# Performance work log

Hardware: AMD Instinct MI355X
Metric: run time of the kernel (lower is better)

Reference implementation:

```python
import jax, jax.numpy as jnp
import numpy as np

N_NODES = 100000


def gcn_conv(x, W, b, src, dst, n_nodes):
    # x: [N, Fin], W: [Fin, Fout], edge (src->dst) with self-loops added,
    # symmetric normalization D^{-1/2} A D^{-1/2} as in PyG GCNConv defaults.
    h = x @ W  # [N, Fout]
    loops = jnp.arange(n_nodes, dtype=src.dtype)
    src_all = jnp.concatenate([src, loops])
    dst_all = jnp.concatenate([dst, loops])
    ones = jnp.ones(src_all.shape[0], dtype=h.dtype)
    deg = jax.ops.segment_sum(ones, dst_all, num_segments=n_nodes)  # in-degree incl. self-loop
    dinv = jnp.where(deg > 0, jax.lax.rsqrt(deg), 0.0)
    norm = dinv[src_all] * dinv[dst_all]  # [E+N]
    msg = h[src_all] * norm[:, None]      # gather + scale
    out = jax.ops.segment_sum(msg, dst_all, num_segments=n_nodes)  # scatter-add
    return out + b


def setup_inputs() -> dict:
    key = jax.random.key(0)
    k1, k2, k3, k4 = jax.random.split(key, 4)
    in_dim, hidden, out_dim = 128, 128, 64
    n_edges = 600000
    x = jax.random.normal(k1, (N_NODES, in_dim), dtype=jnp.float32)
    edge_index = jax.random.randint(k2, (2, n_edges), 0, N_NODES, dtype=jnp.int64)
    # Glorot-ish init for weights
    W1 = jax.random.normal(k3, (in_dim, hidden), dtype=jnp.float32) / np.sqrt(in_dim)
    b1 = jnp.zeros((hidden,), dtype=jnp.float32)
    W2 = jax.random.normal(k4, (hidden, out_dim), dtype=jnp.float32) / np.sqrt(hidden)
    b2 = jnp.zeros((out_dim,), dtype=jnp.float32)
    return {"x": x, "edge_index": edge_index, "W1": W1, "b1": b1, "W2": W2, "b2": b2}


def reference(x, edge_index, W1, b1, W2, b2):
    src, dst = edge_index[0], edge_index[1]
    h = jax.nn.relu(gcn_conv(x, W1, b1, src, dst, N_NODES))
    # dropout is identity in eval mode (training=False)
    return gcn_conv(h, W2, b2, src, dst, N_NODES)
```

## Files before the change

### kernel.cpp

```cpp
#include <hip/hip_runtime.h>
#include <hip/hip_bf16.h>
#include <stdint.h>

typedef unsigned int u32;
typedef unsigned short u16;
typedef unsigned long long u64;
typedef __attribute__((ext_vector_type(8))) short short8;
typedef __attribute__((ext_vector_type(4))) float f32x4;

#define SCAN_TILE 2048

__device__ __forceinline__ float bf2f(u16 u) {
    union { u32 u; float f; } v; v.u = ((u32)u) << 16; return v.f;
}
__device__ __forceinline__ u16 f2bf(float f) {
    u32 u = __float_as_uint(f);
    u32 r = (u + 0x7FFFu + ((u >> 16) & 1u)) >> 16;
    return (u16)r;
}
__device__ __forceinline__ u32 packbf(float lo, float hi) {
    return ((u32)f2bf(hi) << 16) | (u32)f2bf(lo);
}

template<int N>
__device__ __forceinline__ void wpack_one(const void* W, uint4* wpk, int p, int f32w) {
    const int n = p & (N - 1);
    const int kb = p >> ((N == 128) ? 7 : 6);
    u32 pk[4];
    if (f32w) {
        const float* wp = (const float*)W + (size_t)(kb * 8) * N + n;
        #pragma unroll
        for (int jj = 0; jj < 4; jj++)
            pk[jj] = packbf(wp[(2 * jj) * N], wp[(2 * jj + 1) * N]);
    } else {
        const u16* wp = (const u16*)W + (size_t)(kb * 8) * N + n;
        #pragma unroll
        for (int jj = 0; jj < 4; jj++)
            pk[jj] = ((u32)wp[(2 * jj + 1) * N] << 16) | (u32)wp[(2 * jj) * N];
    }
    uint4 v; v.x = pk[0]; v.y = pk[1]; v.z = pk[2]; v.w = pk[3];
    wpk[p] = v;
}

__global__ __launch_bounds__(256) void prep_count_k(
    const u32* __restrict__ xw, const void* __restrict__ ei,
    int* __restrict__ flags, int M, int E,
    const void* __restrict__ W1, const void* __restrict__ W2,
    uint4* __restrict__ wpk1, uint4* __restrict__ wpk2,
    int* __restrict__ deg)
{
    __shared__ int cnt;
    __shared__ u32 orr;
    __shared__ u32 dorr;
    const int b = blockIdx.x, t = threadIdx.x;
    const u32* ew = (const u32*)ei;

    if (b < 12) {
        if (t == 0) cnt = 0;
        __syncthreads();
        int hits = 0;
        #pragma unroll
        for (int j = 0; j < 4; j++) {
            u32 f = (xw[t * 4 + j] >> 7) & 0xFFu;
            if (f >= 100u && f <= 140u) hits++;
        }
        atomicAdd(&cnt, hits);
        __syncthreads();
        const int f32w = (cnt < 512) ? 1 : 0;
        if (b < 8) wpack_one<128>(W1, wpk1, b * 256 + t, f32w);
        else       wpack_one<64> (W2, wpk2, (b - 8) * 256 + t, f32w);
        if (b == 0) {
            if (t == 0) flags[0] = f32w;
            if (t == 0) orr = 0u;
            __syncthreads();
            atomicOr(&orr, ew[2 * t + 1]);
            __syncthreads();
            if (t == 0) flags[1] = (orr == 0u) ? 1 : 0;
        }
        return;
    }

    const int cb = b - 12;
    const int i2 = (cb * 256 + t) * 2;
    if (t == 0) dorr = 0u;
    __syncthreads();
    u32 w = 0u;
    if (i2 + 1 < E) w = ew[(size_t)E + i2 + 1];
    atomicOr(&dorr, w);
    __syncthreads();
    const bool is64 = (dorr == 0u);
    if (i2 >= E) return;
    if (is64) {
        const long long* dp = (const long long*)ei + E;
        if (i2 + 1 < E) {
            longlong2 v = *(const longlong2*)(dp + i2);
            atomicAdd(&deg[(int)v.x], 1);
            atomicAdd(&deg[(int)v.y], 1);
        } else atomicAdd(&deg[(int)dp[i2]], 1);
    } else {
        const int* dp = (const int*)ei + E;
        if (i2 + 1 < E) {
            int2 v = *(const int2*)(dp + i2);
            atomicAdd(&deg[v.x], 1);
            atomicAdd(&deg[v.y], 1);
        } else atomicAdd(&deg[dp[i2]], 1);
    }
}

__global__ __launch_bounds__(256) void scan_gemm1_k(
    const int* __restrict__ deg, int M,
    u64* __restrict__ lk, int* __restrict__ off,
    int* __restrict__ cursor, float* __restrict__ dinv, int nb,
    const void* __restrict__ X, const uint4* __restrict__ wpk,
    u16* __restrict__ HS, const int* __restrict__ flags)
{
    __shared__ u32 smem[64 * 64];
    const int t = threadIdx.x;

    if ((int)blockIdx.x < nb) {
        const int bid = blockIdx.x;
        const int base = bid * SCAN_TILE + t * 8;
        int v[8];
        int s = 0;
        const bool full = (base + 8 <= M);
        if (full) {
            int4 a = *(const int4*)(deg + base);
            int4 b = *(const int4*)(deg + base + 4);
            v[0] = a.x; v[1] = a.y; v[2] = a.z; v[3] = a.w;
            v[4] = b.x; v[5] = b.y; v[6] = b.z; v[7] = b.w;
            s = v[0] + v[1] + v[2] + v[3] + v[4] + v[5] + v[6] + v[7];
        } else {
            #pragma unroll
            for (int j = 0; j < 8; j++) { v[j] = (base + j < M) ? deg[base + j] : 0; s += v[j]; }
        }
        int* bp = (int*)smem;
        int* bq = (int*)smem + 256;
        int* psb = (int*)smem + 512;
        bp[t] = s;
        __syncthreads();
        for (int d = 1; d < 256; d <<= 1) {
            int x = bp[t];
            if (t >= d) x += bp[t - d];
            bq[t] = x;
            __syncthreads();
            int* tmp = bp; bp = bq; bq = tmp;
        }
        const int incl = bp[t];
        const int btotal = bp[255];

        if (t == 0) {
            if (bid == 0) {
                __hip_atomic_store(&lk[0], (2ull << 62) | (u32)btotal,
                                   __ATOMIC_RELEASE, __HIP_MEMORY_SCOPE_AGENT);
                psb[0] = 0;
            } else {
                __hip_atomic_store(&lk[bid], (1ull << 62) | (u32)btotal,
                                   __ATOMIC_RELEASE, __HIP_MEMORY_SCOPE_AGENT);
                int run = 0;
                int j = bid - 1;
                while (j >= 0) {
                    u64 w = __hip_atomic_load(&lk[j], __ATOMIC_ACQUIRE,
                                              __HIP_MEMORY_SCOPE_AGENT);
                    const u64 st = w >> 62;
                    if (st == 0) { __builtin_amdgcn_s_sleep(1); continue; }
                    run += (int)(w & 0xFFFFFFFFull);
                    if (st == 2ull) break;
                    j--;
                }
                psb[0] = run;
                __hip_atomic_store(&lk[bid], (2ull << 62) | (u32)(run + btotal),
                                   __ATOMIC_RELEASE, __HIP_MEMORY_SCOPE_AGENT);
            }
        }
        __syncthreads();
        const int sbase = psb[0];

        int pre = sbase + incl - s;
        int o[8]; float dv[8];
        #pragma unroll
        for (int j = 0; j < 8; j++) {
            o[j] = pre;
            dv[j] = rsqrtf((float)(v[j] + 1));
            pre += v[j];
        }
        if (full) {
            *(int4*)(off + base)     = make_int4(o[0], o[1], o[2], o[3]);
            *(int4*)(off + base + 4) = make_int4(o[4], o[5], o[6], o[7]);
            *(int4*)(cursor + base)     = make_int4(o[0], o[1], o[2], o[3]);
            *(int4*)(cursor + base + 4) = make_int4(o[4], o[5], o[6], o[7]);
            *(float4*)(dinv + base)     = make_float4(dv[0], dv[1], dv[2], dv[3]);
            *(float4*)(dinv + base + 4) = make_float4(dv[4], dv[5], dv[6], dv[7]);
        } else {
            for (int j = 0; j < 8; j++) if (base + j < M) {
                off[base + j] = o[j]; cursor[base + j] = o[j]; dinv[base + j] = dv[j];
            }
        }
        if (bid == nb - 1 && t == 255) off[M] = sbase + btotal;
        return;
    }

    const int gb = (int)blockIdx.x - nb;
    const int wave = t >> 6, lane = t & 63;
    const int q = lane >> 4, m = lane & 15;
    const bool xf32 = (flags[0] != 0);
    const int row0 = gb * 64;
    u32* xlds = smem;

    for (int c = t; c < 1024; c += 256) {
        const int row = c >> 4, c8 = c & 15;
        const int grow = row0 + row;
        uint4 pk = make_uint4(0u, 0u, 0u, 0u);
        if (grow < M) {
            if (xf32) {
                const float* xp = (const float*)X + (size_t)grow * 128 + c8 * 8;
                float4 u = *(const float4*)xp;
                float4 v = *(const float4*)(xp + 4);
                pk.x = packbf(u.x, u.y); pk.y = packbf(u.z, u.w);
                pk.z = packbf(v.x, v.y); pk.w = packbf(v.z, v.w);
            } else {
                pk = *(const uint4*)((const u16*)X + (size_t)grow * 128 + c8 * 8);
            }
        }
        *(uint4*)&xlds[row * 64 + c8 * 4] = pk;
    }
    __syncthreads();

    union { uint4 u; short8 v; } a[4];
    #pragma unroll
    for (int s = 0; s < 4; s++)
        a[s].u = *(const uint4*)&xlds[(wave * 16 + m) * 64 + (s * 4 + q) * 4];

    f32x4 acc[8];
    #pragma unroll
    for (int tt = 0; tt < 8; tt++)
        acc[tt] = (f32x4){0.f, 0.f, 0.f, 0.f};

    #pragma unroll
    for (int s = 0; s < 4; s++) {
        union { uint4 u; short8 v; } b[8];
        #pragma unroll
        for (int tt = 0; tt < 8; tt++)
            b[tt].u = wpk[(s * 4 + q) * 128 + tt * 16 + m];
        #pragma unroll
        for (int tt = 0; tt < 8; tt++)
            acc[tt] = __builtin_amdgcn_mfma_f32_16x16x32_bf16(
                a[s].v, b[tt].v, acc[tt], 0, 0, 0);
    }

    u16* orow = (u16*)&xlds[wave * 16 * 64];
    #pragma unroll
    for (int tt = 0; tt < 8; tt++)
        #pragma unroll
        for (int r = 0; r < 4; r++)
            orow[(q * 4 + r) * 128 + tt * 16 + m] = f2bf(acc[tt][r]);

    #pragma unroll
    for (int j = 0; j < 4; j++) {
        const int cc = lane + j * 64;
        const int lrow = cc >> 4, c8 = cc & 15;
        const int grow = row0 + wave * 16 + lrow;
        uint4 v = *(const uint4*)&((const u32*)orow)[lrow * 64 + c8 * 4];
        if (grow < M)
            *(uint4*)(HS + (size_t)grow * 128 + c8 * 8) = v;
    }
}

__global__ __launch_bounds__(256) void fill_k(const void* __restrict__ ei, int E,
                                              const int* __restrict__ flags,
                                              int* __restrict__ cursor, int* __restrict__ eidx) {
    const int i2 = (blockIdx.x * 256 + threadIdx.x) * 2;
    if (i2 >= E) return;
    int s0, d0, s1 = -1, d1 = -1;
    bool two = (i2 + 1 < E);
    if (flags[1]) {
        const long long* sp = (const long long*)ei;
        const long long* dp = sp + E;
        if (two) {
            longlong2 sv = *(const longlong2*)(sp + i2);
            longlong2 dv = *(const longlong2*)(dp + i2);
            s0 = (int)sv.x; s1 = (int)sv.y; d0 = (int)dv.x; d1 = (int)dv.y;
        } else { s0 = (int)sp[i2]; d0 = (int)dp[i2]; }
    } else {
        const int* sp = (const int*)ei;
        const int* dp = sp + E;
        if (two) {
            int2 sv = *(const int2*)(sp + i2);
            int2 dv = *(const int2*)(dp + i2);
            s0 = sv.x; s1 = sv.y; d0 = dv.x; d1 = dv.y;
        } else { s0 = sp[i2]; d0 = dp[i2]; }
    }
    int p0 = atomicAdd(&cursor[d0], 1);
    eidx[p0] = s0;
    if (two) {
        int p1 = atomicAdd(&cursor[d1], 1);
        eidx[p1] = s1;
    }
}

__global__ __launch_bounds__(256) void agg1_gemm2_k(
    const u16* __restrict__ hs, const int* __restrict__ eidx,
    const int* __restrict__ off, const float* __restrict__ dinv,
    const void* __restrict__ bias, const uint4* __restrict__ wpk,
    u16* __restrict__ HS2, const int* __restrict__ flags, int M)
{
    __shared__ u32 zlds[64 * 64];
    __shared__ int soff[65];
    __shared__ int elds[768];
    const int t = threadIdx.x;
    const int row0 = blockIdx.x * 64;
    const int f32io = flags[0];

    for (int i = t; i <= 64; i += 256) soff[i] = off[min(row0 + i, M)];
    __syncthreads();
    const int beg64 = soff[0];
    const int tot = soff[64] - beg64;
    const bool useLds = (tot <= 768);
    if (useLds) for (int i = t; i < tot; i += 256) elds[i] = eidx[beg64 + i];
    __syncthreads();

    const int lane16 = t & 15, nsub = t >> 4;
    const int c8 = lane16 * 8;
    const u16* __restrict__ hrow = hs + c8;

    float bb[8];
    if (f32io) {
        float4 u = *(const float4*)((const float*)bias + c8);
        float4 v = *(const float4*)((const float*)bias + c8 + 4);
        bb[0] = u.x; bb[1] = u.y; bb[2] = u.z; bb[3] = u.w;
        bb[4] = v.x; bb[5] = v.y; bb[6] = v.z; bb[7] = v.w;
    } else {
        uint4 u = *(const uint4*)((const u16*)bias + c8);
        const u16* s = (const u16*)&u;
        #pragma unroll
        for (int j = 0; j < 8; j++) bb[j] = bf2f(s[j]);
    }

    float acc[4][8]; float dvn[4]; int p[4], e[4];
    #pragma unroll
    for (int r = 0; r < 4; r++) {
        const int li = r * 16 + nsub;
        const int nd = row0 + li;
        const bool ok = nd < M;
        p[r] = soff[li] - beg64;
        e[r] = soff[li + 1] - beg64;
        dvn[r] = ok ? dinv[nd] : 0.f;
        uint4 sp = make_uint4(0u, 0u, 0u, 0u);
        if (ok) sp = *(const uint4*)(hrow + (size_t)nd * 128);
        const u16* s = (const u16*)&sp;
        #pragma unroll
        for (int j = 0; j < 8; j++) acc[r][j] = dvn[r] * bf2f(s[j]);
    }

    while (true) {
        bool any = false;
        #pragma unroll
        for (int r = 0; r < 4; r++) any = any || (p[r] < e[r]);
        if (!any) break;
        int sidx[4]; bool act[4];
        #pragma unroll
        for (int r = 0; r < 4; r++) {
            act[r] = p[r] < e[r];
            const int ip = act[r] ? p[r] : 0;
            sidx[r] = useLds ? elds[ip] : eidx[beg64 + ip];
            p[r] += act[r] ? 1 : 0;
        }
        float dsv[4]; uint4 vv[4];
        #pragma unroll
        for (int r = 0; r < 4; r++) {
            dsv[r] = act[r] ? dinv[sidx[r]] : 0.f;
            vv[r] = *(const uint4*)(hrow + (size_t)sidx[r] * 128);
        }
        #pragma unroll
        for (int r = 0; r < 4; r++) {
            const u16* q = (const u16*)&vv[r];
            #pragma unroll
            for (int j = 0; j < 8; j++)
                acc[r][j] = fmaf(dsv[r], bf2f(q[j]), acc[r][j]);
        }
    }

    #pragma unroll
    for (int r = 0; r < 4; r++) {
        const int li = r * 16 + nsub;
        const int nd = row0 + li;
        float o[8];
        #pragma unroll
        for (int j = 0; j < 8; j++)
            o[j] = (nd < M) ? fmaxf(fmaf(dvn[r], acc[r][j], bb[j]), 0.f) : 0.f;
        uint4 pk;
        pk.x = packbf(o[0], o[1]); pk.y = packbf(o[2], o[3]);
        pk.z = packbf(o[4], o[5]); pk.w = packbf(o[6], o[7]);
        *(uint4*)&zlds[li * 64 + lane16 * 4] = pk;
    }
    __syncthreads();

    const int wave = t >> 6, lane = t & 63;
    const int q = lane >> 4, m = lane & 15;

    union { uint4 u; short8 v; } af[4];
    #pragma unroll
    for (int s = 0; s < 4; s++)
        af[s].u = *(const uint4*)&zlds[(wave * 16 + m) * 64 + (s * 4 + q) * 4];

    f32x4 acg[4];
    #pragma unroll
    for (int tt = 0; tt < 4; tt++)
        acg[tt] = (f32x4){0.f, 0.f, 0.f, 0.f};

    #pragma unroll
    for (int s = 0; s < 4; s++) {
        union { uint4 u; short8 v; } bf_[4];
        #pragma unroll
        for (int tt = 0; tt < 4; tt++)
            bf_[tt].u = wpk[(s * 4 + q) * 64 + tt * 16 + m];
        #pragma unroll
        for (int tt = 0; tt < 4; tt++)
            acg[tt] = __builtin_amdgcn_mfma_f32_16x16x32_bf16(
                af[s].v, bf_[tt].v, acg[tt], 0, 0, 0);
    }

    float dv4[4];
    #pragma unroll
    for (int r = 0; r < 4; r++) {
        const int grow = row0 + wave * 16 + q * 4 + r;
        dv4[r] = (grow < M) ? dinv[grow] : 0.f;
    }

    u16* orow = (u16*)&zlds[wave * 16 * 64];
    __syncthreads();
    #pragma unroll
    for (int tt = 0; tt < 4; tt++)
        #pragma unroll
        for (int r = 0; r < 4; r++)
            orow[(q * 4 + r) * 64 + tt * 16 + m] = f2bf(acg[tt][r] * dv4[r]);

    #pragma unroll
    for (int j = 0; j < 2; j++) {
        const int cc = lane + j * 64;
        const int lrow = cc >> 3, c8b = cc & 7;
        const int grow = row0 + wave * 16 + lrow;
        uint4 v = *(const uint4*)&((const u32*)orow)[lrow * 32 + c8b * 4];
        if (grow < M)
            *(uint4*)(HS2 + (size_t)grow * 64 + c8b * 8) = v;
    }
}

template<int N, bool RELU>
__global__ __launch_bounds__(256) void aggregate_k(
    const u16* __restrict__ hs, const int* __restrict__ eidx,
    const int* __restrict__ off, const float* __restrict__ dinv,
    const void* __restrict__ bias, void* __restrict__ out,
    const int* __restrict__ flags, int out_is_ext, int M)
{
    constexpr int TPN = N / 8;
    constexpr int NPB = 256 / TPN;
    constexpr int ECAP = NPB * 16;
    __shared__ int soff[NPB + 1];
    __shared__ int elds[ECAP];
    const int t = threadIdx.x;
    const int n0 = blockIdx.x * NPB;

    for (int i = t; i <= NPB; i += 256) soff[i] = off[min(n0 + i, M)];
    __syncthreads();
    const int beg0 = soff[0];
    const int tot = soff[NPB] - beg0;
    const bool useLds = (tot <= ECAP);
    if (useLds) for (int i = t; i < tot; i += 256) elds[i] = eidx[beg0 + i];
    __syncthreads();

    const int node = n0 + t / TPN;
    const int lane = t % TPN;
    if (node >= M) return;
    const int f32io = flags[0];
    int p = soff[t / TPN] - beg0;
    const int e = soff[t / TPN + 1] - beg0;
    const int c8 = lane * 8;
    const u16* __restrict__ hrow = hs + c8;

    float a[8];
    {
        uint4 sp = *(const uint4*)(hrow + (size_t)node * N);
        const u16* s = (const u16*)&sp;
        #pragma unroll
        for (int j = 0; j < 8; j++) a[j] = bf2f(s[j]);
    }

    for (; p + 4 <= e; p += 4) {
        int s0, s1, s2, s3;
        if (useLds) { s0 = elds[p]; s1 = elds[p + 1]; s2 = elds[p + 2]; s3 = elds[p + 3]; }
        else { s0 = eidx[beg0 + p]; s1 = eidx[beg0 + p + 1]; s2 = eidx[beg0 + p + 2]; s3 = eidx[beg0 + p + 3]; }
        uint4 v0 = *(const uint4*)(hrow + (size_t)s0 * N);
        uint4 v1 = *(const uint4*)(hrow + (size_t)s1 * N);
        uint4 v2 = *(const uint4*)(hrow + (size_t)s2 * N);
        uint4 v3 = *(const uint4*)(hrow + (size_t)s3 * N);
        const u16* q0 = (const u16*)&v0; const u16* q1 = (const u16*)&v1;
        const u16* q2 = (const u16*)&v2; const u16* q3 = (const u16*)&v3;
        #pragma unroll
        for (int j = 0; j < 8; j++)
            a[j] += (bf2f(q0[j]) + bf2f(q1[j])) + (bf2f(q2[j]) + bf2f(q3[j]));
    }
    for (; p < e; p++) {
        const int s = useLds ? elds[p] : eidx[beg0 + p];
        uint4 v = *(const uint4*)(hrow + (size_t)s * N);
        const u16* q = (const u16*)&v;
        #pragma unroll
        for (int j = 0; j < 8; j++) a[j] += bf2f(q[j]);
    }

    const float dv = dinv[node];
    float b[8];
    if (f32io) {
        float4 u = *(const float4*)((const float*)bias + c8);
        float4 v = *(const float4*)((const float*)bias + c8 + 4);
        b[0] = u.x; b[1] = u.y; b[2] = u.z; b[3] = u.w;
        b[4] = v.x; b[5] = v.y; b[6] = v.z; b[7] = v.w;
    } else {
        uint4 u = *(const uint4*)((const u16*)bias + c8);
        const u16* s = (const u16*)&u;
        #pragma unroll
        for (int j = 0; j < 8; j++) b[j] = bf2f(s[j]);
    }
    float o[8];
    #pragma unroll
    for (int j = 0; j < 8; j++) {
        o[j] = fmaf(dv, a[j], b[j]);
        if (RELU) o[j] = fmaxf(o[j], 0.f);
    }
    if (out_is_ext && f32io) {
        float* op = (float*)out + (size_t)node * N + c8;
        *(float4*)op       = make_float4(o[0], o[1], o[2], o[3]);
        *(float4*)(op + 4) = make_float4(o[4], o[5], o[6], o[7]);
    } else {
        uint4 pk;
        pk.x = packbf(o[0], o[1]); pk.y = packbf(o[2], o[3]);
        pk.z = packbf(o[4], o[5]); pk.w = packbf(o[6], o[7]);
        *(uint4*)((u16*)out + (size_t)node * N + c8) = pk;
    }
}

extern "C" void kernel_launch(void* const* d_in, const int* in_sizes, int n_in,
                              void* d_out, int out_size, void* d_ws, size_t ws_size,
                              hipStream_t stream) {
    const void* x  = d_in[0];
    const void* ei = d_in[1];
    const void* W1 = d_in[2];
    const void* b1 = d_in[3];
    const void* W2 = d_in[4];
    const void* b2 = d_in[5];

    const int M = in_sizes[0] / 128;
    const int E = in_sizes[1] / 2;
    const int NB = (M + SCAN_TILE - 1) / SCAN_TILE;
    const int GB = (M + 63) / 64;
    const int CB = (E + 511) / 512;

    char* ws = (char*)d_ws;
    size_t offb = 0;
    auto alloc = [&](size_t bytes) -> void* {
        void* p = ws + offb; offb += (bytes + 255) & ~(size_t)255; return p;
    };
    int*   flags  = (int*)  alloc(256);
    u64*   lk     = (u64*)  alloc(2048);
    int*   deg    = (int*)  alloc((size_t)M * 4);
    uint4* wpk1   = (uint4*)alloc(16 * 128 * 16);
    uint4* wpk2   = (uint4*)alloc(16 * 64 * 16);
    int*   off    = (int*)  alloc((size_t)(M + 1) * 4);
    int*   cursor = (int*)  alloc((size_t)M * 4);
    float* dinv   = (float*)alloc((size_t)M * 4);
    int*   eidx   = (int*)  alloc((size_t)E * 4);
    u16*   hs1    = (u16*)  alloc((size_t)M * 128 * 2);
    u16*   hs2    = (u16*)  alloc((size_t)M * 64 * 2);
    (void)ws_size; (void)n_in; (void)out_size;

    hipMemsetAsync(lk, 0, 2048 + (size_t)M * 4, stream);
    prep_count_k<<<12 + CB, 256, 0, stream>>>((const u32*)x, ei, flags, M, E,
                                              W1, W2, wpk1, wpk2, deg);
    scan_gemm1_k<<<NB + GB, 256, 0, stream>>>(deg, M, lk, off, cursor, dinv, NB,
                                              x, wpk1, hs1, flags);
    fill_k<<<CB, 256, 0, stream>>>(ei, E, flags, cursor, eidx);
    agg1_gemm2_k<<<GB, 256, 0, stream>>>(hs1, eidx, off, dinv, b1, wpk2, hs2,
                                         flags, M);
    aggregate_k<64, false><<<(M + 31) / 32, 256, 0, stream>>>(hs2, eidx, off, dinv, b2, d_out,
                                                              flags, 1, M);
}
```

Baseline: 230.9 us.

## Split neighbor gathers across wave slots with dynamic node queue in aggregation kernels

Both aggregation kernels now assign one wave per destination node. The node's edge list is split across four 16-lane slots, the partial sums are reduced with cross-lane shuffles, and waves pull the next node from an LDS atomic work queue. Block tiles shrink from 64 to 32 nodes, and the layer-2 GEMM is split so each wave computes half the output columns for a 16-row tile. The layer-2 aggregation uses 4 features per lane instead of 8. This aims to fix load imbalance from skewed degrees and raise memory-level parallelism. The cost is extra shuffles, idle slots on low-degree nodes, and a smaller per-block GEMM.

```diff
diff --git a/kernel.cpp b/kernel.cpp
--- a/kernel.cpp
+++ b/kernel.cpp
@@ -303,22 +303,25 @@
     const void* __restrict__ bias, const uint4* __restrict__ wpk,
     u16* __restrict__ HS2, const int* __restrict__ flags, int M)
 {
-    __shared__ u32 zlds[64 * 64];
-    __shared__ int soff[65];
-    __shared__ int elds[768];
+    __shared__ u32 zlds[32 * 64];
+    __shared__ int soff[33];
+    __shared__ int elds[512];
+    __shared__ int wq;
     const int t = threadIdx.x;
-    const int row0 = blockIdx.x * 64;
+    const int row0 = blockIdx.x * 32;
     const int f32io = flags[0];
 
-    for (int i = t; i <= 64; i += 256) soff[i] = off[min(row0 + i, M)];
-    __syncthreads();
-    const int beg64 = soff[0];
-    const int tot = soff[64] - beg64;
-    const bool useLds = (tot <= 768);
-    if (useLds) for (int i = t; i < tot; i += 256) elds[i] = eidx[beg64 + i];
-    __syncthreads();
-
-    const int lane16 = t & 15, nsub = t >> 4;
+    if (t == 0) wq = 4;
+    for (int i = t; i <= 32; i += 256) soff[i] = off[min(row0 + i, M)];
+    __syncthreads();
+    const int beg0 = soff[0];
+    const int tot = soff[32] - beg0;
+    const bool useLds = (tot <= 512);
+    if (useLds) for (int i = t; i < tot; i += 256) elds[i] = eidx[beg0 + i];
+    __syncthreads();
+
+    const int wave = t >> 6, lane = t & 63;
+    const int lane16 = lane & 15, slot = lane >> 4;
     const int c8 = lane16 * 8;
     const u16* __restrict__ hrow = hs + c8;
 
@@ -335,206 +338,185 @@
         for (int j = 0; j < 8; j++) bb[j] = bf2f(s[j]);
     }
 
-    float acc[4][8]; float dvn[4]; int p[4], e[4];
-    #pragma unroll
-    for (int r = 0; r < 4; r++) {
-        const int li = r * 16 + nsub;
-        const int nd = row0 + li;
-        const bool ok = nd < M;
-        p[r] = soff[li] - beg64;
-        e[r] = soff[li + 1] - beg64;
-        dvn[r] = ok ? dinv[nd] : 0.f;
-        uint4 sp = make_uint4(0u, 0u, 0u, 0u);
-        if (ok) sp = *(const uint4*)(hrow + (size_t)nd * 128);
-        const u16* s = (const u16*)&sp;
-        #pragma unroll
-        for (int j = 0; j < 8; j++) acc[r][j] = dvn[r] * bf2f(s[j]);
-    }
-
-    while (true) {
-        bool any = false;
-        #pragma unroll
-        for (int r = 0; r < 4; r++) any = any || (p[r] < e[r]);
-        if (!any) break;
-        int sidx[4]; bool act[4];
-        #pragma unroll
-        for (int r = 0; r < 4; r++) {
-            act[r] = p[r] < e[r];
-            const int ip = act[r] ? p[r] : 0;
-            sidx[r] = useLds ? elds[ip] : eidx[beg64 + ip];
-            p[r] += act[r] ? 1 : 0;
-        }
-        float dsv[4]; uint4 vv[4];
-        #pragma unroll
-        for (int r = 0; r < 4; r++) {
-            dsv[r] = act[r] ? dinv[sidx[r]] : 0.f;
-            vv[r] = *(const uint4*)(hrow + (size_t)sidx[r] * 128);
-        }
-        #pragma unroll
-        for (int r = 0; r < 4; r++) {
-            const u16* q = (const u16*)&vv[r];
+    int n = wave;
+    while (n < 32) {
+        const int nd = row0 + n;
+        const int pb = soff[n] - beg0;
+        const int pe = soff[n + 1] - beg0;
+        const float dv = (nd < M) ? dinv[nd] : 0.f;
+        float a[8];
+        #pragma unroll
+        for (int j = 0; j < 8; j++) a[j] = 0.f;
+        if (slot == 0 && nd < M) {
+            uint4 sp = *(const uint4*)(hrow + (size_t)nd * 128);
+            const u16* s = (const u16*)&sp;
+            #pragma unroll
+            for (int j = 0; j < 8; j++) a[j] = dv * bf2f(s[j]);
+        }
+        for (int p = pb; p < pe; p += 4) {
+            const int ip = p + slot;
+            if (ip < pe) {
+                const int s = useLds ? elds[ip] : eidx[beg0 + ip];
+                const float ds = dinv[s];
+                uint4 v = *(const uint4*)(hrow + (size_t)s * 128);
+                const u16* q = (const u16*)&v;
+                #pragma unroll
+                for (int j = 0; j < 8; j++) a[j] = fmaf(ds, bf2f(q[j]), a[j]);
+            }
+        }
+        #pragma unroll
+        for (int j = 0; j < 8; j++) {
+            a[j] += __shfl_xor(a[j], 16);
+            a[j] += __shfl_xor(a[j], 32);
+        }
+        if (slot == 0) {
+            float o[8];
             #pragma unroll
             for (int j = 0; j < 8; j++)
-                acc[r][j] = fmaf(dsv[r], bf2f(q[j]), acc[r][j]);
-        }
-    }
-
+                o[j] = (nd < M) ? fmaxf(fmaf(dv, a[j], bb[j]), 0.f) : 0.f;
+            uint4 pk;
+            pk.x = packbf(o[0], o[1]); pk.y = packbf(o[2], o[3]);
+            pk.z = packbf(o[4], o[5]); pk.w = packbf(o[6], o[7]);
+            *(uint4*)&zlds[n * 64 + lane16 * 4] = pk;
+        }
+        if (lane == 0) n = atomicAdd(&wq, 1);
+        n = __shfl(n, 0);
+    }
+    __syncthreads();
+
+    const int q = lane >> 4, m = lane & 15;
+    const int mt = wave >> 1, nh = wave & 1;
+
+    union { uint4 u; short8 v; } af[4];
+    #pragma unroll
+    for (int s = 0; s < 4; s++)
+        af[s].u = *(const uint4*)&zlds[(mt * 16 + m) * 64 + (s * 4 + q) * 4];
+
+    f32x4 acg[2];
+    #pragma unroll
+    for (int u = 0; u < 2; u++)
+        acg[u] = (f32x4){0.f, 0.f, 0.f, 0.f};
+
+    #pragma unroll
+    for (int s = 0; s < 4; s++) {
+        union { uint4 u; short8 v; } bf_[2];
+        #pragma unroll
+        for (int u = 0; u < 2; u++)
+            bf_[u].u = wpk[(s * 4 + q) * 64 + (nh * 2 + u) * 16 + m];
+        #pragma unroll
+        for (int u = 0; u < 2; u++)
+            acg[u] = __builtin_amdgcn_mfma_f32_16x16x32_bf16(
+                af[s].v, bf_[u].v, acg[u], 0, 0, 0);
+    }
+
+    float dvq[4];
     #pragma unroll
     for (int r = 0; r < 4; r++) {
-        const int li = r * 16 + nsub;
-        const int nd = row0 + li;
-        float o[8];
-        #pragma unroll
-        for (int j = 0; j < 8; j++)
-            o[j] = (nd < M) ? fmaxf(fmaf(dvn[r], acc[r][j], bb[j]), 0.f) : 0.f;
-        uint4 pk;
-        pk.x = packbf(o[0], o[1]); pk.y = packbf(o[2], o[3]);
-        pk.z = packbf(o[4], o[5]); pk.w = packbf(o[6], o[7]);
-        *(uint4*)&zlds[li * 64 + lane16 * 4] = pk;
-    }
-    __syncthreads();
-
-    const int wave = t >> 6, lane = t & 63;
-    const int q = lane >> 4, m = lane & 15;
-
-    union { uint4 u; short8 v; } af[4];
-    #pragma unroll
-    for (int s = 0; s < 4; s++)
-        af[s].u = *(const uint4*)&zlds[(wave * 16 + m) * 64 + (s * 4 + q) * 4];
-
-    f32x4 acg[4];
-    #pragma unroll
-    for (int tt = 0; tt < 4; tt++)
-        acg[tt] = (f32x4){0.f, 0.f, 0.f, 0.f};
-
-    #pragma unroll
-    for (int s = 0; s < 4; s++) {
-        union { uint4 u; short8 v; } bf_[4];
-        #pragma unroll
-        for (int tt = 0; tt < 4; tt++)
-            bf_[tt].u = wpk[(s * 4 + q) * 64 + tt * 16 + m];
-        #pragma unroll
-        for (int tt = 0; tt < 4; tt++)
-            acg[tt] = __builtin_amdgcn_mfma_f32_16x16x32_bf16(
-                af[s].v, bf_[tt].v, acg[tt], 0, 0, 0);
-    }
-
-    float dv4[4];
-    #pragma unroll
-    for (int r = 0; r < 4; r++) {
-        const int grow = row0 + wave * 16 + q * 4 + r;
-        dv4[r] = (grow < M) ? dinv[grow] : 0.f;
-    }
-
-    u16* orow = (u16*)&zlds[wave * 16 * 64];
-    __syncthreads();
-    #pragma unroll
-    for (int tt = 0; tt < 4; tt++)
+        const int grow = row0 + mt * 16 + q * 4 + r;
+        dvq[r] = (grow < M) ? dinv[grow] : 0.f;
+    }
+
+    __syncthreads();
+    u16* orow = (u16*)&zlds[wave * 256];
+    #pragma unroll
+    for (int u = 0; u < 2; u++)
         #pragma unroll
         for (int r = 0; r < 4; r++)
-            orow[(q * 4 + r) * 64 + tt * 16 + m] = f2bf(acg[tt][r] * dv4[r]);
-
-    #pragma unroll
-    for (int j = 0; j < 2; j++) {
-        const int cc = lane + j * 64;
-        const int lrow = cc >> 3, c8b = cc & 7;
-        const int grow = row0 + wave * 16 + lrow;
-        uint4 v = *(const uint4*)&((const u32*)orow)[lrow * 32 + c8b * 4];
+            orow[(q * 4 + r) * 32 + u * 16 + m] = f2bf(acg[u][r] * dvq[r]);
+
+    {
+        const int c = lane;
+        const int lrow = c >> 2, c4 = c & 3;
+        const int grow = row0 + mt * 16 + lrow;
+        uint4 v = *(const uint4*)&((const u32*)orow)[lrow * 16 + c4 * 4];
         if (grow < M)
-            *(uint4*)(HS2 + (size_t)grow * 64 + c8b * 8) = v;
-    }
-}
-
-template<int N, bool RELU>
-__global__ __launch_bounds__(256) void aggregate_k(
+            *(uint4*)(HS2 + (size_t)grow * 64 + nh * 32 + c4 * 8) = v;
+    }
+}
+
+__global__ __launch_bounds__(256) void agg2_k(
     const u16* __restrict__ hs, const int* __restrict__ eidx,
     const int* __restrict__ off, const float* __restrict__ dinv,
     const void* __restrict__ bias, void* __restrict__ out,
-    const int* __restrict__ flags, int out_is_ext, int M)
+    const int* __restrict__ flags, int M)
 {
-    constexpr int TPN = N / 8;
-    constexpr int NPB = 256 / TPN;
-    constexpr int ECAP = NPB * 16;
-    __shared__ int soff[NPB + 1];
-    __shared__ int elds[ECAP];
+    __shared__ int soff[33];
+    __shared__ int elds[512];
+    __shared__ int wq;
     const int t = threadIdx.x;
-    const int n0 = blockIdx.x * NPB;
-
-    for (int i = t; i <= NPB; i += 256) soff[i] = off[min(n0 + i, M)];
+    const int n0 = blockIdx.x * 32;
+    const int f32io = flags[0];
+
+    if (t == 0) wq = 4;
+    for (int i = t; i <= 32; i += 256) soff[i] = off[min(n0 + i, M)];
     __syncthreads();
     const int beg0 = soff[0];
-    const int tot = soff[NPB] - beg0;
-    const bool useLds = (tot <= ECAP);
+    const int tot = soff[32] - beg0;
+    const bool useLds = (tot <= 512);
     if (useLds) for (int i = t; i < tot; i += 256) elds[i] = eidx[beg0 + i];
     __syncthreads();
 
-    const int node = n0 + t / TPN;
-    const int lane = t % TPN;
-    if (node >= M) return;
-    const int f32io = flags[0];
-    int p = soff[t / TPN] - beg0;
-    const int e = soff[t / TPN + 1] - beg0;
-    const int c8 = lane * 8;
-    const u16* __restrict__ hrow = hs + c8;
-
-    float a[8];
-    {
-        uint4 sp = *(const uint4*)(hrow + (size_t)node * N);
-        const u16* s = (const u16*)&sp;
-        #pragma unroll
-        for (int j = 0; j < 8; j++) a[j] = bf2f(s[j]);
-    }
-
-    for (; p + 4 <= e; p += 4) {
-        int s0, s1, s2, s3;
-        if (useLds) { s0 = elds[p]; s1 = elds[p + 1]; s2 = elds[p + 2]; s3 = elds[p + 3]; }
-        else { s0 = eidx[beg0 + p]; s1 = eidx[beg0 + p + 1]; s2 = eidx[beg0 + p + 2]; s3 = eidx[beg0 + p + 3]; }
-        uint4 v0 = *(const uint4*)(hrow + (size_t)s0 * N);
-        uint4 v1 = *(const uint4*)(hrow + (size_t)s1 * N);
-        uint4 v2 = *(const uint4*)(hrow + (size_t)s2 * N);
-        uint4 v3 = *(const uint4*)(hrow + (size_t)s3 * N);
-        const u16* q0 = (const u16*)&v0; const u16* q1 = (const u16*)&v1;
-        const u16* q2 = (const u16*)&v2; const u16* q3 = (const u16*)&v3;
-        #pragma unroll
-        for (int j = 0; j < 8; j++)
-            a[j] += (bf2f(q0[j]) + bf2f(q1[j])) + (bf2f(q2[j]) + bf2f(q3[j]));
-    }
-    for (; p < e; p++) {
-        const int s = useLds ? elds[p] : eidx[beg0 + p];
-        uint4 v = *(const uint4*)(hrow + (size_t)s * N);
-        const u16* q = (const u16*)&v;
-        #pragma unroll
-        for (int j = 0; j < 8; j++) a[j] += bf2f(q[j]);
-    }
-
-    const float dv = dinv[node];
-    float b[8];
+    const int wave = t >> 6, lane = t & 63;
+    const int lane16 = lane & 15, slot = lane >> 4;
+    const int c4 = lane16 * 4;
+    const u16* __restrict__ hrow = hs + c4;
+
+    float bb[4];
     if (f32io) {
-        float4 u = *(const float4*)((const float*)bias + c8);
-        float4 v = *(const float4*)((const float*)bias + c8 + 4);
-        b[0] = u.x; b[1] = u.y; b[2] = u.z; b[3] = u.w;
-        b[4] = v.x; b[5] = v.y; b[6] = v.z; b[7] = v.w;
+        float4 u = *(const float4*)((const float*)bias + c4);
+        bb[0] = u.x; bb[1] = u.y; bb[2] = u.z; bb[3] = u.w;
     } else {
-        uint4 u = *(const uint4*)((const u16*)bias + c8);
+        uint2 u = *(const uint2*)((const u16*)bias + c4);
         const u16* s = (const u16*)&u;
         #pragma unroll
-        for (int j = 0; j < 8; j++) b[j] = bf2f(s[j]);
-    }
-    float o[8];
-    #pragma unroll
-    for (int j = 0; j < 8; j++) {
-        o[j] = fmaf(dv, a[j], b[j]);
-        if (RELU) o[j] = fmaxf(o[j], 0.f);
-    }
-    if (out_is_ext && f32io) {
-        float* op = (float*)out + (size_t)node * N + c8;
-        *(float4*)op       = make_float4(o[0], o[1], o[2], o[3]);
-        *(float4*)(op + 4) = make_float4(o[4], o[5], o[6], o[7]);
-    } else {
-        uint4 pk;
-        pk.x = packbf(o[0], o[1]); pk.y = packbf(o[2], o[3]);
-        pk.z = packbf(o[4], o[5]); pk.w = packbf(o[6], o[7]);
-        *(uint4*)((u16*)out + (size_t)node * N + c8) = pk;
+        for (int j = 0; j < 4; j++) bb[j] = bf2f(s[j]);
+    }
+
+    int n = wave;
+    while (n < 32) {
+        const int nd = n0 + n;
+        const int pb = soff[n] - beg0;
+        const int pe = soff[n + 1] - beg0;
+        float a[4];
+        #pragma unroll
+        for (int j = 0; j < 4; j++) a[j] = 0.f;
+        if (slot == 0 && nd < M) {
+            uint2 sp = *(const uint2*)(hrow + (size_t)nd * 64);
+            const u16* s = (const u16*)&sp;
+            #pragma unroll
+            for (int j = 0; j < 4; j++) a[j] = bf2f(s[j]);
+        }
+        for (int p = pb; p < pe; p += 4) {
+            const int ip = p + slot;
+            if (ip < pe) {
+                const int s = useLds ? elds[ip] : eidx[beg0 + ip];
+                uint2 v = *(const uint2*)(hrow + (size_t)s * 64);
+                const u16* q = (const u16*)&v;
+                #pragma unroll
+                for (int j = 0; j < 4; j++) a[j] += bf2f(q[j]);
+            }
+        }
+        #pragma unroll
+        for (int j = 0; j < 4; j++) {
+            a[j] += __shfl_xor(a[j], 16);
+            a[j] += __shfl_xor(a[j], 32);
+        }
+        if (slot == 0 && nd < M) {
+            const float dv = dinv[nd];
+            float o[4];
+            #pragma unroll
+            for (int j = 0; j < 4; j++) o[j] = fmaf(dv, a[j], bb[j]);
+            if (f32io) {
+                *(float4*)((float*)out + (size_t)nd * 64 + c4) =
+                    make_float4(o[0], o[1], o[2], o[3]);
+            } else {
+                uint2 pk;
+                pk.x = packbf(o[0], o[1]); pk.y = packbf(o[2], o[3]);
+                *(uint2*)((u16*)out + (size_t)nd * 64 + c4) = pk;
+            }
+        }
+        if (lane == 0) n = atomicAdd(&wq, 1);
+        n = __shfl(n, 0);
     }
 }
 
@@ -578,8 +560,8 @@
     scan_gemm1_k<<<NB + GB, 256, 0, stream>>>(deg, M, lk, off, cursor, dinv, NB,
                                               x, wpk1, hs1, flags);
     fill_k<<<CB, 256, 0, stream>>>(ei, E, flags, cursor, eidx);
-    agg1_gemm2_k<<<GB, 256, 0, stream>>>(hs1, eidx, off, dinv, b1, wpk2, hs2,
-                                         flags, M);
-    aggregate_k<64, false><<<(M + 31) / 32, 256, 0, stream>>>(hs2, eidx, off, dinv, b2, d_out,
-                                                              flags, 1, M);
-}
+    agg1_gemm2_k<<<(M + 31) / 32, 256, 0, stream>>>(hs1, eidx, off, dinv, b1, wpk2, hs2,
+                                                    flags, M);
+    agg2_k<<<(M + 31) / 32, 256, 0, stream>>>(hs2, eidx, off, dinv, b2, d_out,
+                                              flags, M);
+}
```

Result: slower. 246.1 us (+6.6%).

## Move GEMM1 from scan kernel into fill kernel launch

Applied to the files above, without the earlier changes.

The decoupled-lookback scan becomes its own small kernel. The first GEMM now shares a launch with the CSR fill, not with the scan. The intent is to keep the serial lookback chain from sharing the GPU with heavy GEMM blocks, and to overlap the atomic-bound fill with the compute-bound GEMM instead. The number of launches stays the same, but the scan now runs alone, and the fill and GEMM blocks compete for the same CUs.

```diff
diff --git a/kernel.cpp b/kernel.cpp
--- a/kernel.cpp
+++ b/kernel.cpp
@@ -107,104 +107,136 @@
     }
 }
 
-__global__ __launch_bounds__(256) void scan_gemm1_k(
-    const int* __restrict__ deg, int M,
-    u64* __restrict__ lk, int* __restrict__ off,
-    int* __restrict__ cursor, float* __restrict__ dinv, int nb,
+__global__ __launch_bounds__(256) void scan_lb_k(const int* __restrict__ deg, int M,
+                                                 u64* __restrict__ lk,
+                                                 int* __restrict__ off,
+                                                 int* __restrict__ cursor,
+                                                 float* __restrict__ dinv, int nb) {
+    const int bid = blockIdx.x, t = threadIdx.x;
+    const int base = bid * SCAN_TILE + t * 8;
+    int v[8];
+    int s = 0;
+    const bool full = (base + 8 <= M);
+    if (full) {
+        int4 a = *(const int4*)(deg + base);
+        int4 b = *(const int4*)(deg + base + 4);
+        v[0] = a.x; v[1] = a.y; v[2] = a.z; v[3] = a.w;
+        v[4] = b.x; v[5] = b.y; v[6] = b.z; v[7] = b.w;
+        s = v[0] + v[1] + v[2] + v[3] + v[4] + v[5] + v[6] + v[7];
+    } else {
+        #pragma unroll
+        for (int j = 0; j < 8; j++) { v[j] = (base + j < M) ? deg[base + j] : 0; s += v[j]; }
+    }
+    __shared__ int buf[2][256];
+    buf[0][t] = s;
+    __syncthreads();
+    int cur = 0;
+    for (int d = 1; d < 256; d <<= 1) {
+        int x = buf[cur][t];
+        if (t >= d) x += buf[cur][t - d];
+        buf[cur ^ 1][t] = x;
+        __syncthreads();
+        cur ^= 1;
+    }
+    const int incl = buf[cur][t];
+    const int btotal = buf[cur][255];
+
+    __shared__ int sbase;
+    if (t == 0) {
+        if (bid == 0) {
+            __hip_atomic_store(&lk[0], (2ull << 62) | (u32)btotal,
+                               __ATOMIC_RELEASE, __HIP_MEMORY_SCOPE_AGENT);
+            sbase = 0;
+        } else {
+            __hip_atomic_store(&lk[bid], (1ull << 62) | (u32)btotal,
+                               __ATOMIC_RELEASE, __HIP_MEMORY_SCOPE_AGENT);
+            int run = 0;
+            int j = bid - 1;
+            while (j >= 0) {
+                u64 w = __hip_atomic_load(&lk[j], __ATOMIC_ACQUIRE,
+                                          __HIP_MEMORY_SCOPE_AGENT);
+                const u64 st = w >> 62;
+                if (st == 0) { __builtin_amdgcn_s_sleep(1); continue; }
+                run += (int)(w & 0xFFFFFFFFull);
+                if (st == 2ull) break;
+                j--;
+            }
+            sbase = run;
+            __hip_atomic_store(&lk[bid], (2ull << 62) | (u32)(run + btotal),
+                               __ATOMIC_RELEASE, __HIP_MEMORY_SCOPE_AGENT);
+        }
+    }
+    __syncthreads();
+
+    int pre = sbase + incl - s;
+    int o[8]; float dv[8];
+    #pragma unroll
+    for (int j = 0; j < 8; j++) {
+        o[j] = pre;
+        dv[j] = rsqrtf((float)(v[j] + 1));
+        pre += v[j];
+    }
+    if (full) {
+        *(int4*)(off + base)     = make_int4(o[0], o[1], o[2], o[3]);
+        *(int4*)(off + base + 4) = make_int4(o[4], o[5], o[6], o[7]);
+        *(int4*)(cursor + base)     = make_int4(o[0], o[1], o[2], o[3]);
+        *(int4*)(cursor + base + 4) = make_int4(o[4], o[5], o[6], o[7]);
+        *(float4*)(dinv + base)     = make_float4(dv[0], dv[1], dv[2], dv[3]);
+        *(float4*)(dinv + base + 4) = make_float4(dv[4], dv[5], dv[6], dv[7]);
+    } else {
+        for (int j = 0; j < 8; j++) if (base + j < M) {
+            off[base + j] = o[j]; cursor[base + j] = o[j]; dinv[base + j] = dv[j];
+        }
+    }
+    if (bid == nb - 1 && t == 255) off[M] = sbase + btotal;
+}
+
+__global__ __launch_bounds__(256) void fill_gemm1_k(
+    const void* __restrict__ ei, int E,
+    const int* __restrict__ flags,
+    int* __restrict__ cursor, int* __restrict__ eidx, int nf,
     const void* __restrict__ X, const uint4* __restrict__ wpk,
-    u16* __restrict__ HS, const int* __restrict__ flags)
+    u16* __restrict__ HS, int M)
 {
-    __shared__ u32 smem[64 * 64];
+    __shared__ u32 xlds[64 * 64];
     const int t = threadIdx.x;
 
-    if ((int)blockIdx.x < nb) {
-        const int bid = blockIdx.x;
-        const int base = bid * SCAN_TILE + t * 8;
-        int v[8];
-        int s = 0;
-        const bool full = (base + 8 <= M);
-        if (full) {
-            int4 a = *(const int4*)(deg + base);
-            int4 b = *(const int4*)(deg + base + 4);
-            v[0] = a.x; v[1] = a.y; v[2] = a.z; v[3] = a.w;
-            v[4] = b.x; v[5] = b.y; v[6] = b.z; v[7] = b.w;
-            s = v[0] + v[1] + v[2] + v[3] + v[4] + v[5] + v[6] + v[7];
+    if ((int)blockIdx.x < nf) {
+        const int i2 = ((int)blockIdx.x * 256 + t) * 2;
+        if (i2 >= E) return;
+        int s0, d0, s1 = -1, d1 = -1;
+        bool two = (i2 + 1 < E);
+        if (flags[1]) {
+            const long long* sp = (const long long*)ei;
+            const long long* dp = sp + E;
+            if (two) {
+                longlong2 sv = *(const longlong2*)(sp + i2);
+                longlong2 dv = *(const longlong2*)(dp + i2);
+                s0 = (int)sv.x; s1 = (int)sv.y; d0 = (int)dv.x; d1 = (int)dv.y;
+            } else { s0 = (int)sp[i2]; d0 = (int)dp[i2]; }
         } else {
-            #pragma unroll
-            for (int j = 0; j < 8; j++) { v[j] = (base + j < M) ? deg[base + j] : 0; s += v[j]; }
-        }
-        int* bp = (int*)smem;
-        int* bq = (int*)smem + 256;
-        int* psb = (int*)smem + 512;
-        bp[t] = s;
-        __syncthreads();
-        for (int d = 1; d < 256; d <<= 1) {
-            int x = bp[t];
-            if (t >= d) x += bp[t - d];
-            bq[t] = x;
-            __syncthreads();
-            int* tmp = bp; bp = bq; bq = tmp;
-        }
-        const int incl = bp[t];
-        const int btotal = bp[255];
-
-        if (t == 0) {
-            if (bid == 0) {
-                __hip_atomic_store(&lk[0], (2ull << 62) | (u32)btotal,
-                                   __ATOMIC_RELEASE, __HIP_MEMORY_SCOPE_AGENT);
-                psb[0] = 0;
-            } else {
-                __hip_atomic_store(&lk[bid], (1ull << 62) | (u32)btotal,
-                                   __ATOMIC_RELEASE, __HIP_MEMORY_SCOPE_AGENT);
-                int run = 0;
-                int j = bid - 1;
-                while (j >= 0) {
-                    u64 w = __hip_atomic_load(&lk[j], __ATOMIC_ACQUIRE,
-                                              __HIP_MEMORY_SCOPE_AGENT);
-                    const u64 st = w >> 62;
-                    if (st == 0) { __builtin_amdgcn_s_sleep(1); continue; }
-                    run += (int)(w & 0xFFFFFFFFull);
-                    if (st == 2ull) break;
-                    j--;
-                }
-                psb[0] = run;
-                __hip_atomic_store(&lk[bid], (2ull << 62) | (u32)(run + btotal),
-                                   __ATOMIC_RELEASE, __HIP_MEMORY_SCOPE_AGENT);
-            }
-        }
-        __syncthreads();
-        const int sbase = psb[0];
-
-        int pre = sbase + incl - s;
-        int o[8]; float dv[8];
-        #pragma unroll
-        for (int j = 0; j < 8; j++) {
-            o[j] = pre;
-            dv[j] = rsqrtf((float)(v[j] + 1));
-            pre += v[j];
-        }
-        if (full) {
-            *(int4*)(off + base)     = make_int4(o[0], o[1], o[2], o[3]);
-            *(int4*)(off + base + 4) = make_int4(o[4], o[5], o[6], o[7]);
-            *(int4*)(cursor + base)     = make_int4(o[0], o[1], o[2], o[3]);
-            *(int4*)(cursor + base + 4) = make_int4(o[4], o[5], o[6], o[7]);
-            *(float4*)(dinv + base)     = make_float4(dv[0], dv[1], dv[2], dv[3]);
-            *(float4*)(dinv + base + 4) = make_float4(dv[4], dv[5], dv[6], dv[7]);
-        } else {
-            for (int j = 0; j < 8; j++) if (base + j < M) {
-                off[base + j] = o[j]; cursor[base + j] = o[j]; dinv[base + j] = dv[j];
-            }
-        }
-        if (bid == nb - 1 && t == 255) off[M] = sbase + btotal;
+            const int* sp = (const int*)ei;
+            const int* dp = sp + E;
+            if (two) {
+                int2 sv = *(const int2*)(sp + i2);
+                int2 dv = *(const int2*)(dp + i2);
+                s0 = sv.x; s1 = sv.y; d0 = dv.x; d1 = dv.y;
+            } else { s0 = sp[i2]; d0 = dp[i2]; }
+        }
+        int p0 = atomicAdd(&cursor[d0], 1);
+        eidx[p0] = s0;
+        if (two) {
+            int p1 = atomicAdd(&cursor[d1], 1);
+            eidx[p1] = s1;
+        }
         return;
     }
 
-    const int gb = (int)blockIdx.x - nb;
+    const int gb = (int)blockIdx.x - nf;
     const int wave = t >> 6, lane = t & 63;
     const int q = lane >> 4, m = lane & 15;
     const bool xf32 = (flags[0] != 0);
     const int row0 = gb * 64;
-    u32* xlds = smem;
 
     for (int c = t; c < 1024; c += 256) {
         const int row = c >> 4, c8 = c & 15;
@@ -262,38 +294,6 @@
         uint4 v = *(const uint4*)&((const u32*)orow)[lrow * 64 + c8 * 4];
         if (grow < M)
             *(uint4*)(HS + (size_t)grow * 128 + c8 * 8) = v;
-    }
-}
-
-__global__ __launch_bounds__(256) void fill_k(const void* __restrict__ ei, int E,
-                                              const int* __restrict__ flags,
-                                              int* __restrict__ cursor, int* __restrict__ eidx) {
-    const int i2 = (blockIdx.x * 256 + threadIdx.x) * 2;
-    if (i2 >= E) return;
-    int s0, d0, s1 = -1, d1 = -1;
-    bool two = (i2 + 1 < E);
-    if (flags[1]) {
-        const long long* sp = (const long long*)ei;
-        const long long* dp = sp + E;
-        if (two) {
-            longlong2 sv = *(const longlong2*)(sp + i2);
-            longlong2 dv = *(const longlong2*)(dp + i2);
-            s0 = (int)sv.x; s1 = (int)sv.y; d0 = (int)dv.x; d1 = (int)dv.y;
-        } else { s0 = (int)sp[i2]; d0 = (int)dp[i2]; }
-    } else {
-        const int* sp = (const int*)ei;
-        const int* dp = sp + E;
-        if (two) {
-            int2 sv = *(const int2*)(sp + i2);
-            int2 dv = *(const int2*)(dp + i2);
-            s0 = sv.x; s1 = sv.y; d0 = dv.x; d1 = dv.y;
-        } else { s0 = sp[i2]; d0 = dp[i2]; }
-    }
-    int p0 = atomicAdd(&cursor[d0], 1);
-    eidx[p0] = s0;
-    if (two) {
-        int p1 = atomicAdd(&cursor[d1], 1);
-        eidx[p1] = s1;
     }
 }
 
@@ -575,9 +575,9 @@
     hipMemsetAsync(lk, 0, 2048 + (size_t)M * 4, stream);
     prep_count_k<<<12 + CB, 256, 0, stream>>>((const u32*)x, ei, flags, M, E,
                                               W1, W2, wpk1, wpk2, deg);
-    scan_gemm1_k<<<NB + GB, 256, 0, stream>>>(deg, M, lk, off, cursor, dinv, NB,
-                                              x, wpk1, hs1, flags);
-    fill_k<<<CB, 256, 0, stream>>>(ei, E, flags, cursor, eidx);
+    scan_lb_k<<<NB, 256, 0, stream>>>(deg, M, lk, off, cursor, dinv, NB);
+    fill_gemm1_k<<<CB + GB, 256, 0, stream>>>(ei, E, flags, cursor, eidx, CB,
+                                              x, wpk1, hs1, M);
     agg1_gemm2_k<<<GB, 256, 0, stream>>>(hs1, eidx, off, dinv, b1, wpk2, hs2,
                                          flags, M);
     aggregate_k<64, false><<<(M + 31) / 32, 256, 0, stream>>>(hs2, eidx, off, dinv, b2, d_out,
```

Measured after the change: 234.5 us. Within noise of the previous version (+1.5%).
